# Kernel optimization log

Hardware: AMD Instinct MI355X
Metric: run time of the kernel (lower is better)

Reference implementation:

```python
import jax, jax.numpy as jnp
import numpy as np

N_NODES = 100000
N_EDGES = 1600000


def setup_inputs() -> dict:
    key = jax.random.key(0)
    k1, k2, k3, k4 = jax.random.split(key, 4)
    x = jax.random.normal(k1, (N_NODES, 256), dtype=jnp.float32)
    edge_index = jax.random.randint(k2, (2, N_EDGES), 0, N_NODES, dtype=jnp.int64)
    W1 = jax.random.normal(k3, (256, 128), dtype=jnp.float32) * (1.0 / np.sqrt(256))
    W2 = jax.random.normal(k4, (128, 40), dtype=jnp.float32) * (1.0 / np.sqrt(128))
    return {"x": x, "edge_index": edge_index, "W1": W1, "W2": W2}


def _gcn_conv(x, W, src, dst):
    # GCNConv(normalize=False, add_self_loops=False, bias=False):
    # linear transform then sum-aggregate messages along edges src->dst.
    h = x @ W                                   # [N, d_out]
    msg = h[src]                                # [E, d_out] gather
    return jax.ops.segment_sum(msg, dst, num_segments=N_NODES)  # [N, d_out] scatter-add


def reference(x, edge_index, W1, W2):
    src, dst = edge_index[0], edge_index[1]
    h = jax.nn.relu(_gcn_conv(x, W1, src, dst))
    # dropout is identity in eval mode
    out = _gcn_conv(h, W2, src, dst)
    return out
```

## Files before the change

### kernel.cpp

```cpp
#include <hip/hip_runtime.h>

constexpr int NN = 100000;
constexpr int NE = 1600000;
constexpr int DI = 256, DH = 128, DO = 40;

constexpr int NB = (NN + 255) >> 8;
constexpr int NB_BLK = 512;
constexpr int CHUNK = NE / NB_BLK;
constexpr int M2 = NB * NB_BLK;
constexpr int NBS = (M2 + 1023) / 1024;
constexpr int STAGE_CAP = 6144;
constexpr int WPACK_BLOCKS = 152;
constexpr int GEMM1_BLOCKS = (NN + 63) / 64;

typedef __attribute__((ext_vector_type(8))) __bf16 bf16x8;
typedef __attribute__((ext_vector_type(4))) float f32x4;

__device__ inline float4 bf4_to_f4(ushort4 u) {
    return make_float4(__builtin_bit_cast(float, (unsigned)u.x << 16),
                       __builtin_bit_cast(float, (unsigned)u.y << 16),
                       __builtin_bit_cast(float, (unsigned)u.z << 16),
                       __builtin_bit_cast(float, (unsigned)u.w << 16));
}
__device__ inline unsigned short f2bf(float f) {
    return __builtin_bit_cast(unsigned short, (__bf16)f);
}
__device__ inline bf16x8 bf16x8_zero() {
    bf16x8 r;
    #pragma unroll
    for (int j = 0; j < 8; ++j) r[j] = (__bf16)0.f;
    return r;
}
__device__ inline bf16x8 load_cvt_a(const float* __restrict__ p, bool ok) {
    if (!ok) return bf16x8_zero();
    bf16x8 r;
    const float4 v0 = *(const float4*)p;
    const float4 v1 = *(const float4*)(p + 4);
    r[0] = (__bf16)v0.x; r[1] = (__bf16)v0.y; r[2] = (__bf16)v0.z; r[3] = (__bf16)v0.w;
    r[4] = (__bf16)v1.x; r[5] = (__bf16)v1.y; r[6] = (__bf16)v1.z; r[7] = (__bf16)v1.w;
    return r;
}
__device__ inline void acc4(float4& a, float4 v) {
    a.x += v.x; a.y += v.y; a.z += v.z; a.w += v.w;
}

__global__ __launch_bounds__(256) void wpack_hist_kernel(const float* __restrict__ W1,
                                                         const float* __restrict__ W2,
                                                         const int* __restrict__ dst,
                                                         __bf16* __restrict__ Wf,
                                                         __bf16* __restrict__ Wf2,
                                                         int* __restrict__ hist2d) {
    __shared__ int h[NB];
    if (blockIdx.x < 128) {
        const int i = blockIdx.x * 256 + threadIdx.x;
        const int j = i & 7;
        const int lane = (i >> 3) & 63;
        const int nt = (i >> 9) & 7;
        const int kt = i >> 12;
        const int k = kt * 32 + (lane >> 4) * 8 + j;
        const int n = nt * 16 + (lane & 15);
        Wf[i] = (__bf16)W1[(size_t)k * DH + n];
    } else if (blockIdx.x < WPACK_BLOCKS) {
        const int i = (blockIdx.x - 128) * 256 + threadIdx.x;
        if (i < 6144) {
            const int j = i & 7;
            const int lane = (i >> 3) & 63;
            const int g = i >> 9;
            const int nt = g % 3, ks = g / 3;
            const int k = ks * 32 + (lane >> 4) * 8 + j;
            const int n = nt * 16 + (lane & 15);
            Wf2[i] = (n < DO) ? (__bf16)W2[(size_t)k * DO + n] : (__bf16)0.f;
        }
    } else {
        const int hb = blockIdx.x - WPACK_BLOCKS;
        for (int i = threadIdx.x; i < NB; i += 256) h[i] = 0;
        __syncthreads();
        const int base = hb * CHUNK;
        for (int i = threadIdx.x; i < CHUNK; i += 256)
            atomicAdd(&h[dst[base + i] >> 8], 1);
        __syncthreads();
        for (int i = threadIdx.x; i < NB; i += 256)
            hist2d[i * NB_BLK + hb] = h[i];
    }
}

__global__ __launch_bounds__(256) void gemm1_scan_kernel(const float* __restrict__ x,
                                                         const __bf16* __restrict__ Wf,
                                                         __bf16* __restrict__ h1,
                                                         const int* __restrict__ hist2d,
                                                         int* __restrict__ offs2d) {
    __shared__ __bf16 wlds[32768];
    if (blockIdx.x >= NBS) {
        const int t = threadIdx.x;
        const int wave = t >> 6, lane = t & 63;
        const int q = lane >> 4, m = lane & 15;
        const int row0 = (blockIdx.x - NBS) * 64 + wave * 16;
        const int r = row0 + m;
        const bool ok = r < NN;
        const float* xp = x + (size_t)r * DI;

        bf16x8 a[8];
        #pragma unroll
        for (int kt = 0; kt < 8; ++kt)
            a[kt] = load_cvt_a(xp + kt * 32 + q * 8, ok);

        bf16x8* wl = (bf16x8*)wlds;
        const bf16x8* wfv = (const bf16x8*)Wf;
        #pragma unroll
        for (int i = 0; i < 16; ++i)
            wl[t + i * 256] = wfv[t + i * 256];

        f32x4 acc[8];
        #pragma unroll
        for (int nt = 0; nt < 8; ++nt)
            #pragma unroll
            for (int rr = 0; rr < 4; ++rr) acc[nt][rr] = 0.f;

        __syncthreads();

        #pragma unroll
        for (int kt = 0; kt < 8; ++kt) {
            #pragma unroll
            for (int nt = 0; nt < 8; ++nt) {
                const bf16x8 b = wl[(kt * 8 + nt) * 64 + lane];
                acc[nt] = __builtin_amdgcn_mfma_f32_16x16x32_bf16(a[kt], b, acc[nt], 0, 0, 0);
            }
        }
        #pragma unroll
        for (int reg = 0; reg < 4; ++reg) {
            const int rr = row0 + q * 4 + reg;
            if (rr < NN) {
                __bf16* hp = h1 + (size_t)rr * DH + m;
                #pragma unroll
                for (int nt = 0; nt < 8; ++nt) hp[nt * 16] = (__bf16)acc[nt][reg];
            }
        }
    } else {
        int* red = (int*)wlds;
        const int b = blockIdx.x;
        const int t = threadIdx.x;
        int s = 0;
        const int limit = b * 1024;
        for (int i = t * 4; i < limit; i += 1024) {
            const int4 v = *(const int4*)(hist2d + i);
            s += v.x + v.y + v.z + v.w;
        }
        red[t] = s;
        __syncthreads();
        #pragma unroll
        for (int d = 128; d > 0; d >>= 1) {
            if (t < d) red[t] += red[t + d];
            __syncthreads();
        }
        const int base = red[0];
        __syncthreads();
        const int idx = b * 1024 + t * 4;
        int4 v = make_int4(0, 0, 0, 0);
        if (idx < M2) v = *(const int4*)(hist2d + idx);
        const int sl = v.x + v.y + v.z + v.w;
        red[t] = sl;
        __syncthreads();
        for (int d = 1; d < 256; d <<= 1) {
            const int u = (t >= d) ? red[t - d] : 0;
            __syncthreads();
            red[t] += u;
            __syncthreads();
        }
        if (idx < M2) {
            const int e0 = base + red[t] - sl;
            *(int4*)(offs2d + idx) = make_int4(e0, e0 + v.x, e0 + v.x + v.y,
                                               e0 + v.x + v.y + v.z);
        }
    }
}

__global__ __launch_bounds__(256) void bucket_scatter_kernel(const int* __restrict__ src,
                                                             const int* __restrict__ dst,
                                                             const int* __restrict__ offs2d,
                                                             unsigned* __restrict__ epack) {
    __shared__ int cur[NB];
    for (int i = threadIdx.x; i < NB; i += 256)
        cur[i] = offs2d[i * NB_BLK + blockIdx.x];
    __syncthreads();
    const int base = blockIdx.x * CHUNK;
    for (int i = threadIdx.x; i < CHUNK; i += 256) {
        const int d = dst[base + i], s = src[base + i];
        const int p = atomicAdd(&cur[d >> 8], 1);
        epack[p] = (unsigned)s | ((unsigned)(d & 255) << 24);
    }
}

__global__ __launch_bounds__(256) void bucket_sort_kernel(const unsigned* __restrict__ epack,
                                                          const int* __restrict__ offs2d,
                                                          int* __restrict__ off,
                                                          int* __restrict__ esrc) {
    __shared__ int cnt[256];
    __shared__ int incl[256];
    __shared__ int cur[256];
    __shared__ int stage[STAGE_CAP];
    const int b = blockIdx.x;
    const int t = threadIdx.x;
    const int bstart = offs2d[b * NB_BLK];
    const int bend = (b + 1 < NB) ? offs2d[(b + 1) * NB_BLK] : NE;
    const int n = bend - bstart;
    cnt[t] = 0;
    __syncthreads();
    for (int i = t; i < n; i += 256)
        atomicAdd(&cnt[epack[bstart + i] >> 24], 1);
    __syncthreads();
    incl[t] = cnt[t];
    __syncthreads();
    for (int d = 1; d < 256; d <<= 1) {
        const int u = (t >= d) ? incl[t - d] : 0;
        __syncthreads();
        incl[t] += u;
        __syncthreads();
    }
    const int ex = incl[t] - cnt[t];
    const int node = (b << 8) + t;
    if (node <= NN) off[node] = bstart + ex;
    cur[t] = ex;
    __syncthreads();
    const bool staged = (n <= STAGE_CAP);
    for (int i = t; i < n; i += 256) {
        const unsigned pk = epack[bstart + i];
        const int p = atomicAdd(&cur[pk >> 24], 1);
        const int s = (int)(pk & 0xFFFFFFu);
        if (staged) stage[p] = s;
        else esrc[bstart + p] = s;
    }
    __syncthreads();
    if (staged)
        for (int i = t; i < n; i += 256) esrc[bstart + i] = stage[i];
}

__global__ __launch_bounds__(256) void agg1g2_kernel(const __bf16* __restrict__ h1,
                                                     const int* __restrict__ esrc,
                                                     const int* __restrict__ off,
                                                     const __bf16* __restrict__ Wf2,
                                                     __bf16* __restrict__ h2) {
    __shared__ __bf16 rows[16][136];
    const int t = threadIdx.x;
    const int wave = t >> 6, lane = t & 63;
    const int half = lane >> 5;
    const int c = (lane & 31) * 4;
    const int node0 = blockIdx.x * 16;

    for (int k = 0; k < 4; ++k) {
        const int r = wave * 4 + k;
        const int w = node0 + r;
        const int b = off[w], e = off[w + 1];
        float4 a0 = make_float4(0.f, 0.f, 0.f, 0.f);
        float4 a1 = a0, a2 = a0, a3 = a0;
        int j = b + half;
        for (; j + 6 < e; j += 8) {
            const int s0 = esrc[j], s1 = esrc[j + 2], s2 = esrc[j + 4], s3 = esrc[j + 6];
            acc4(a0, bf4_to_f4(*(const ushort4*)(h1 + (size_t)s0 * DH + c)));
            acc4(a1, bf4_to_f4(*(const ushort4*)(h1 + (size_t)s1 * DH + c)));
            acc4(a2, bf4_to_f4(*(const ushort4*)(h1 + (size_t)s2 * DH + c)));
            acc4(a3, bf4_to_f4(*(const ushort4*)(h1 + (size_t)s3 * DH + c)));
        }
        for (; j < e; j += 2) {
            const int s = esrc[j];
            acc4(a0, bf4_to_f4(*(const ushort4*)(h1 + (size_t)s * DH + c)));
        }
        float4 acc = make_float4(a0.x + a1.x + a2.x + a3.x,
                                 a0.y + a1.y + a2.y + a3.y,
                                 a0.z + a1.z + a2.z + a3.z,
                                 a0.w + a1.w + a2.w + a3.w);
        acc.x += __shfl_xor(acc.x, 32);
        acc.y += __shfl_xor(acc.y, 32);
        acc.z += __shfl_xor(acc.z, 32);
        acc.w += __shfl_xor(acc.w, 32);
        if (half == 0) {
            ushort4 o;
            o.x = f2bf(fmaxf(acc.x, 0.f));
            o.y = f2bf(fmaxf(acc.y, 0.f));
            o.z = f2bf(fmaxf(acc.z, 0.f));
            o.w = f2bf(fmaxf(acc.w, 0.f));
            *(ushort4*)(&rows[r][c]) = o;
        }
    }
    __syncthreads();

    if (wave < 3) {
        const int nt = wave;
        const int q = lane >> 4, m = lane & 15;
        f32x4 acc;
        #pragma unroll
        for (int rr = 0; rr < 4; ++rr) acc[rr] = 0.f;
        const bf16x8* wf2 = (const bf16x8*)Wf2;
        #pragma unroll
        for (int ks = 0; ks < 4; ++ks) {
            const bf16x8 a = *(const bf16x8*)(&rows[m][ks * 32 + q * 8]);
            const bf16x8 b = wf2[(ks * 3 + nt) * 64 + lane];
            acc = __builtin_amdgcn_mfma_f32_16x16x32_bf16(a, b, acc, 0, 0, 0);
        }
        const int cc = nt * 16 + m;
        if (cc < DO) {
            #pragma unroll
            for (int reg = 0; reg < 4; ++reg) {
                const int rr = node0 + q * 4 + reg;
                h2[(size_t)rr * DO + cc] = (__bf16)acc[reg];
            }
        }
    }
}

__global__ __launch_bounds__(256) void agg2_kernel(const __bf16* __restrict__ h2,
                                                   const int* __restrict__ esrc,
                                                   const int* __restrict__ off,
                                                   float* __restrict__ out) {
    const int w = (blockIdx.x * 256 + threadIdx.x) >> 6;
    if (w >= NN) return;
    const int lane = threadIdx.x & 63;
    const int sub = lane / 10;
    const int c = (lane % 10) * 4;
    const int b = off[w], e = off[w + 1];
    const int deg = e - b;
    float4 a0 = make_float4(0.f, 0.f, 0.f, 0.f);
    float4 a1 = a0, a2 = a0, a3 = a0;

    for (int base = 0; base < deg; base += 64) {
        const int cnt = min(64, deg - base);
        const int cl = cnt - 1;
        const int idx = (base + lane < deg) ? esrc[b + base + lane] : 0;
        const bool act = sub < 6;
        int kk = 0;
        for (; kk + 24 <= cnt; kk += 24) {
            const int e0 = kk + sub;
            const int s0 = __shfl(idx, min(e0, cl));
            const int s1 = __shfl(idx, min(e0 + 6, cl));
            const int s2 = __shfl(idx, min(e0 + 12, cl));
            const int s3 = __shfl(idx, min(e0 + 18, cl));
            const float4 v0 = bf4_to_f4(*(const ushort4*)(h2 + (size_t)s0 * DO + c));
            const float4 v1 = bf4_to_f4(*(const ushort4*)(h2 + (size_t)s1 * DO + c));
            const float4 v2 = bf4_to_f4(*(const ushort4*)(h2 + (size_t)s2 * DO + c));
            const float4 v3 = bf4_to_f4(*(const ushort4*)(h2 + (size_t)s3 * DO + c));
            if (act) { acc4(a0, v0); acc4(a1, v1); acc4(a2, v2); acc4(a3, v3); }
        }
        for (; kk + 12 <= cnt; kk += 12) {
            const int e0 = kk + sub;
            const int s0 = __shfl(idx, min(e0, cl));
            const int s1 = __shfl(idx, min(e0 + 6, cl));
            const float4 v0 = bf4_to_f4(*(const ushort4*)(h2 + (size_t)s0 * DO + c));
            const float4 v1 = bf4_to_f4(*(const ushort4*)(h2 + (size_t)s1 * DO + c));
            if (act) { acc4(a0, v0); acc4(a1, v1); }
        }
        for (; kk < cnt; kk += 6) {
            const int e0 = kk + sub;
            const int s0 = __shfl(idx, min(e0, cl));
            const float4 v = bf4_to_f4(*(const ushort4*)(h2 + (size_t)s0 * DO + c));
            if (act && e0 < cnt) acc4(a0, v);
        }
    }
    float4 acc = make_float4(a0.x + a1.x + a2.x + a3.x, a0.y + a1.y + a2.y + a3.y,
                             a0.z + a1.z + a2.z + a3.z, a0.w + a1.w + a2.w + a3.w);
    acc.x += __shfl(acc.x, lane + 30);
    acc.y += __shfl(acc.y, lane + 30);
    acc.z += __shfl(acc.z, lane + 30);
    acc.w += __shfl(acc.w, lane + 30);
    const float ax = acc.x + __shfl(acc.x, lane + 10) + __shfl(acc.x, lane + 20);
    const float ay = acc.y + __shfl(acc.y, lane + 10) + __shfl(acc.y, lane + 20);
    const float az = acc.z + __shfl(acc.z, lane + 10) + __shfl(acc.z, lane + 20);
    const float aw = acc.w + __shfl(acc.w, lane + 10) + __shfl(acc.w, lane + 20);
    if (lane < 10) {
        *(float4*)(out + (size_t)w * DO + c) = make_float4(ax, ay, az, aw);
    }
}

extern "C" void kernel_launch(void* const* d_in, const int* in_sizes, int n_in,
                              void* d_out, int out_size, void* d_ws, size_t ws_size,
                              hipStream_t stream) {
    const float* x  = (const float*)d_in[0];
    const int*   ei = (const int*)d_in[1];
    const float* W1 = (const float*)d_in[2];
    const float* W2 = (const float*)d_in[3];
    const int* src = ei;
    const int* dst = ei + NE;

    __bf16* Wf  = (__bf16*)d_ws;
    __bf16* Wf2 = Wf + 32768;
    __bf16* h1  = Wf2 + 6144;
    __bf16* h2  = h1 + (size_t)NN * DH;
    unsigned* epack = (unsigned*)(h2 + (size_t)NN * DO);
    int* esrc   = (int*)(epack + NE);
    int* off    = esrc + NE;
    int* hist2d = off + NN + 1;
    int* offs2d = hist2d + M2;

    float* out = (float*)d_out;

    wpack_hist_kernel<<<WPACK_BLOCKS + NB_BLK, 256, 0, stream>>>(W1, W2, dst, Wf, Wf2, hist2d);
    gemm1_scan_kernel<<<GEMM1_BLOCKS + NBS, 256, 0, stream>>>(x, Wf, h1, hist2d, offs2d);
    bucket_scatter_kernel<<<NB_BLK, 256, 0, stream>>>(src, dst, offs2d, epack);
    bucket_sort_kernel<<<NB, 256, 0, stream>>>(epack, offs2d, off, esrc);
    agg1g2_kernel<<<NN / 16, 256, 0, stream>>>(h1, esrc, off, Wf2, h2);
    agg2_kernel<<<(NN * 64 + 255) / 256, 256, 0, stream>>>(h2, esrc, off, out);
}
```

Baseline: 329.6 us.

## Pad h2 rows to 64 bf16 and gather 16-byte vectors in layer-2 aggregation

```diff
diff --git a/kernel.cpp b/kernel.cpp
--- a/kernel.cpp
+++ b/kernel.cpp
@@ -3,6 +3,7 @@
 constexpr int NN = 100000;
 constexpr int NE = 1600000;
 constexpr int DI = 256, DH = 128, DO = 40;
+constexpr int DP = 64;
 
 constexpr int NB = (NN + 255) >> 8;
 constexpr int NB_BLK = 512;
@@ -15,6 +16,7 @@
 
 typedef __attribute__((ext_vector_type(8))) __bf16 bf16x8;
 typedef __attribute__((ext_vector_type(4))) float f32x4;
+typedef __attribute__((ext_vector_type(8))) unsigned short u16x8;
 
 __device__ inline float4 bf4_to_f4(ushort4 u) {
     return make_float4(__builtin_bit_cast(float, (unsigned)u.x << 16),
@@ -42,6 +44,11 @@
 }
 __device__ inline void acc4(float4& a, float4 v) {
     a.x += v.x; a.y += v.y; a.z += v.z; a.w += v.w;
+}
+__device__ inline void acc8(float* a, u16x8 v) {
+    #pragma unroll
+    for (int i = 0; i < 8; ++i)
+        a[i] += __builtin_bit_cast(float, (unsigned)v[i] << 16);
 }
 
 __global__ __launch_bounds__(256) void wpack_hist_kernel(const float* __restrict__ W1,
@@ -283,9 +290,9 @@
     }
     __syncthreads();
 
+    const int q = lane >> 4, m = lane & 15;
     if (wave < 3) {
         const int nt = wave;
-        const int q = lane >> 4, m = lane & 15;
         f32x4 acc;
         #pragma unroll
         for (int rr = 0; rr < 4; ++rr) acc[rr] = 0.f;
@@ -297,12 +304,16 @@
             acc = __builtin_amdgcn_mfma_f32_16x16x32_bf16(a, b, acc, 0, 0, 0);
         }
         const int cc = nt * 16 + m;
-        if (cc < DO) {
-            #pragma unroll
-            for (int reg = 0; reg < 4; ++reg) {
-                const int rr = node0 + q * 4 + reg;
-                h2[(size_t)rr * DO + cc] = (__bf16)acc[reg];
-            }
+        #pragma unroll
+        for (int reg = 0; reg < 4; ++reg) {
+            const int rr = node0 + q * 4 + reg;
+            h2[(size_t)rr * DP + cc] = (__bf16)((cc < DO) ? acc[reg] : 0.f);
+        }
+    } else {
+        #pragma unroll
+        for (int reg = 0; reg < 4; ++reg) {
+            const int rr = node0 + q * 4 + reg;
+            h2[(size_t)rr * DP + 48 + m] = (__bf16)0.f;
         }
     }
 }
@@ -314,58 +325,34 @@
     const int w = (blockIdx.x * 256 + threadIdx.x) >> 6;
     if (w >= NN) return;
     const int lane = threadIdx.x & 63;
-    const int sub = lane / 10;
-    const int c = (lane % 10) * 4;
+    const int sub = lane >> 3;
+    const int c = (lane & 7) * 8;
     const int b = off[w], e = off[w + 1];
-    const int deg = e - b;
-    float4 a0 = make_float4(0.f, 0.f, 0.f, 0.f);
-    float4 a1 = a0, a2 = a0, a3 = a0;
-
-    for (int base = 0; base < deg; base += 64) {
-        const int cnt = min(64, deg - base);
-        const int cl = cnt - 1;
-        const int idx = (base + lane < deg) ? esrc[b + base + lane] : 0;
-        const bool act = sub < 6;
-        int kk = 0;
-        for (; kk + 24 <= cnt; kk += 24) {
-            const int e0 = kk + sub;
-            const int s0 = __shfl(idx, min(e0, cl));
-            const int s1 = __shfl(idx, min(e0 + 6, cl));
-            const int s2 = __shfl(idx, min(e0 + 12, cl));
-            const int s3 = __shfl(idx, min(e0 + 18, cl));
-            const float4 v0 = bf4_to_f4(*(const ushort4*)(h2 + (size_t)s0 * DO + c));
-            const float4 v1 = bf4_to_f4(*(const ushort4*)(h2 + (size_t)s1 * DO + c));
-            const float4 v2 = bf4_to_f4(*(const ushort4*)(h2 + (size_t)s2 * DO + c));
-            const float4 v3 = bf4_to_f4(*(const ushort4*)(h2 + (size_t)s3 * DO + c));
-            if (act) { acc4(a0, v0); acc4(a1, v1); acc4(a2, v2); acc4(a3, v3); }
-        }
-        for (; kk + 12 <= cnt; kk += 12) {
-            const int e0 = kk + sub;
-            const int s0 = __shfl(idx, min(e0, cl));
-            const int s1 = __shfl(idx, min(e0 + 6, cl));
-            const float4 v0 = bf4_to_f4(*(const ushort4*)(h2 + (size_t)s0 * DO + c));
-            const float4 v1 = bf4_to_f4(*(const ushort4*)(h2 + (size_t)s1 * DO + c));
-            if (act) { acc4(a0, v0); acc4(a1, v1); }
-        }
-        for (; kk < cnt; kk += 6) {
-            const int e0 = kk + sub;
-            const int s0 = __shfl(idx, min(e0, cl));
-            const float4 v = bf4_to_f4(*(const ushort4*)(h2 + (size_t)s0 * DO + c));
-            if (act && e0 < cnt) acc4(a0, v);
-        }
-    }
-    float4 acc = make_float4(a0.x + a1.x + a2.x + a3.x, a0.y + a1.y + a2.y + a3.y,
-                             a0.z + a1.z + a2.z + a3.z, a0.w + a1.w + a2.w + a3.w);
-    acc.x += __shfl(acc.x, lane + 30);
-    acc.y += __shfl(acc.y, lane + 30);
-    acc.z += __shfl(acc.z, lane + 30);
-    acc.w += __shfl(acc.w, lane + 30);
-    const float ax = acc.x + __shfl(acc.x, lane + 10) + __shfl(acc.x, lane + 20);
-    const float ay = acc.y + __shfl(acc.y, lane + 10) + __shfl(acc.y, lane + 20);
-    const float az = acc.z + __shfl(acc.z, lane + 10) + __shfl(acc.z, lane + 20);
-    const float aw = acc.w + __shfl(acc.w, lane + 10) + __shfl(acc.w, lane + 20);
-    if (lane < 10) {
-        *(float4*)(out + (size_t)w * DO + c) = make_float4(ax, ay, az, aw);
+    float a0[8] = {0.f, 0.f, 0.f, 0.f, 0.f, 0.f, 0.f, 0.f};
+    float a1[8] = {0.f, 0.f, 0.f, 0.f, 0.f, 0.f, 0.f, 0.f};
+    int j = b + sub;
+    for (; j + 8 < e; j += 16) {
+        const int s0 = esrc[j], s1 = esrc[j + 8];
+        const u16x8 v0 = *(const u16x8*)(h2 + (size_t)s0 * DP + c);
+        const u16x8 v1 = *(const u16x8*)(h2 + (size_t)s1 * DP + c);
+        acc8(a0, v0); acc8(a1, v1);
+    }
+    for (; j < e; j += 8) {
+        const u16x8 v = *(const u16x8*)(h2 + (size_t)esrc[j] * DP + c);
+        acc8(a0, v);
+    }
+    float r[8];
+    #pragma unroll
+    for (int i = 0; i < 8; ++i) r[i] = a0[i] + a1[i];
+    #pragma unroll
+    for (int i = 0; i < 8; ++i) r[i] += __shfl_xor(r[i], 8);
+    #pragma unroll
+    for (int i = 0; i < 8; ++i) r[i] += __shfl_xor(r[i], 16);
+    #pragma unroll
+    for (int i = 0; i < 8; ++i) r[i] += __shfl_xor(r[i], 32);
+    if (sub == 0 && c < DO) {
+        *(float4*)(out + (size_t)w * DO + c) = make_float4(r[0], r[1], r[2], r[3]);
+        *(float4*)(out + (size_t)w * DO + c + 4) = make_float4(r[4], r[5], r[6], r[7]);
     }
 }
 
@@ -383,7 +370,7 @@
     __bf16* Wf2 = Wf + 32768;
     __bf16* h1  = Wf2 + 6144;
     __bf16* h2  = h1 + (size_t)NN * DH;
-    unsigned* epack = (unsigned*)(h2 + (size_t)NN * DO);
+    unsigned* epack = (unsigned*)(h2 + (size_t)NN * DP);
     int* esrc   = (int*)(epack + NE);
     int* off    = esrc + NE;
     int* hist2d = off + NN + 1;
```

Result: no change. 332.3 us (+0.8%).
